# Kernel optimization log

Hardware: AMD Instinct MI355X
Metric: run time of the kernel (lower is better)

Reference implementation:

```python
import jax, jax.numpy as jnp
import numpy as np

EPS = 1e-5


def _bn(v, gamma, beta, mean, var):
    # v: [n, c, L, 1]; per-channel eval-mode batchnorm
    scale = gamma / jnp.sqrt(var + EPS)
    return v * scale[None, :, None, None] + (beta - mean * scale)[None, :, None, None]


def _conv1x1(v, w, b):
    # v: [n, c, L, 1], w: [o, c], b: [o] -> [n, o, L, 1]
    y = jnp.einsum('ncl,oc->nol', v[..., 0], w) + b[None, :, None]
    return y[..., None]


def setup_inputs() -> dict:
    key = jax.random.key(0)
    ks = jax.random.split(key, 16)
    N, C, H, W, MIP = 8, 256, 112, 112, 8
    return {
        'x': jax.random.normal(ks[0], (N, C, H, W), dtype=jnp.float32),
        'bn1_gamma': jax.random.uniform(ks[1], (C,), dtype=jnp.float32),
        'bn1_beta': jax.random.normal(ks[2], (C,), dtype=jnp.float32) * 0.1,
        'bn1_mean': jax.random.normal(ks[3], (C,), dtype=jnp.float32) * 0.1,
        'bn1_var': jax.random.uniform(ks[4], (C,), dtype=jnp.float32) + 0.5,
        'bn2_gamma': jax.random.uniform(ks[5], (C,), dtype=jnp.float32),
        'bn2_beta': jax.random.normal(ks[6], (C,), dtype=jnp.float32) * 0.1,
        'bn2_mean': jax.random.normal(ks[7], (C,), dtype=jnp.float32) * 0.1,
        'bn2_var': jax.random.uniform(ks[8], (C,), dtype=jnp.float32) + 0.5,
        'ds_w': jax.random.normal(ks[9], (MIP, C), dtype=jnp.float32) * (1.0 / np.sqrt(C)),
        'ds_b': jax.random.normal(ks[10], (MIP,), dtype=jnp.float32) * 0.01,
        'us_w': jax.random.normal(ks[11], (C, MIP), dtype=jnp.float32) * (1.0 / np.sqrt(MIP)),
        'us_b': jax.random.normal(ks[12], (C,), dtype=jnp.float32) * 0.01,
    }


def reference(x, bn1_gamma, bn1_beta, bn1_mean, bn1_var,
              bn2_gamma, bn2_beta, bn2_mean, bn2_var,
              ds_w, ds_b, us_w, us_b):
    identity = x
    # dual-axis average pooling
    x_h = jnp.mean(x, axis=3, keepdims=True)                 # [n, c, h, 1]
    x_w = jnp.mean(x, axis=2, keepdims=True).transpose(0, 1, 3, 2)  # [n, c, w, 1]
    # batchnorm (eval mode)
    x_h = _bn(x_h, bn1_gamma, bn1_beta, bn1_mean, bn1_var)
    x_w = _bn(x_w, bn2_gamma, bn2_beta, bn2_mean, bn2_var)
    # channel-reduce 1x1 conv + relu
    d_h = jax.nn.relu(_conv1x1(x_h, ds_w, ds_b))             # [n, mip, h, 1]
    d_w = jax.nn.relu(_conv1x1(x_w, ds_w, ds_b))             # [n, mip, w, 1]
    # channel-expand 1x1 conv + sigmoid
    a_h = jax.nn.sigmoid(_conv1x1(d_h, us_w, us_b))          # [n, c, h, 1]
    a_w = jax.nn.sigmoid(_conv1x1(d_w, us_w, us_b))          # [n, c, w, 1]
    a_w = a_w.transpose(0, 1, 3, 2)                          # [n, c, 1, w]
    out = identity * a_w * a_h + identity
    # h_swish: x * relu6(x + 3) / 6
    return out * jnp.clip(out + 3.0, 0.0, 6.0) * (1.0 / 6.0)
```

## Files before the change

kernel.cpp:

```cpp
#include <hip/hip_runtime.h>
#include <math.h>

#define NN 8
#define CC 256
#define HH 112
#define WW 112
#define MIP 8
#define EPS 1e-5f

__global__ __launch_bounds__(128) void pool_kernel(const float* __restrict__ x,
                                                   float* __restrict__ pool) {
    const int b = blockIdx.x;
    const int tid = threadIdx.x;
    const float* plane = x + (size_t)b * (HH * WW);

    if (tid < WW) {
        float s = 0.f;
#pragma unroll 4
        for (int h = 0; h < HH; ++h) s += plane[h * WW + tid];
        pool[(size_t)(NN * CC * HH) + (size_t)b * WW + tid] = s * (1.0f / HH);
    }
    if (tid < HH) {
        float s = 0.f;
#pragma unroll 4
        for (int w = 0; w < WW; ++w) s += plane[tid * WW + w];
        pool[(size_t)b * HH + tid] = s * (1.0f / WW);
    }
}

__global__ __launch_bounds__(256) void att_kernel(
    float* __restrict__ pool,
    const float* __restrict__ bn1_g, const float* __restrict__ bn1_b,
    const float* __restrict__ bn1_m, const float* __restrict__ bn1_v,
    const float* __restrict__ bn2_g, const float* __restrict__ bn2_b,
    const float* __restrict__ bn2_m, const float* __restrict__ bn2_v,
    const float* __restrict__ ds_w, const float* __restrict__ ds_b,
    const float* __restrict__ us_w, const float* __restrict__ us_b) {
    __shared__ float s[CC];
    __shared__ float dsh[MIP];

    const int n = blockIdx.x / HH;
    const int pos = blockIdx.x % HH;
    const int branch = blockIdx.y;
    const int c = threadIdx.x;

    const float* g  = branch ? bn2_g : bn1_g;
    const float* be = branch ? bn2_b : bn1_b;
    const float* mn = branch ? bn2_m : bn1_m;
    const float* vr = branch ? bn2_v : bn1_v;

    const size_t base = (size_t)branch * (NN * CC * HH);
    const size_t idx = base + ((size_t)(n * CC + c)) * HH + pos;

    float v = pool[idx];
    float scale = g[c] * rsqrtf(vr[c] + EPS);
    float vb = v * scale + (be[c] - mn[c] * scale);
    s[c] = vb;
    __syncthreads();

    {
        const int grp = c >> 5;
        const int l = c & 31;
        float partial = 0.f;
#pragma unroll
        for (int k = 0; k < CC / 32; ++k) {
            const int cc = l + k * 32;
            partial += ds_w[grp * CC + cc] * s[cc];
        }
#pragma unroll
        for (int off = 16; off > 0; off >>= 1)
            partial += __shfl_down(partial, off, 32);
        if (l == 0) dsh[grp] = fmaxf(partial + ds_b[grp], 0.f);
    }
    __syncthreads();

    float acc = us_b[c];
#pragma unroll
    for (int m = 0; m < MIP; ++m) acc += us_w[c * MIP + m] * dsh[m];
    float a = 1.0f / (1.0f + expf(-acc));
    pool[idx] = a;
}

__global__ __launch_bounds__(256) void apply_kernel(const float* __restrict__ x,
                                                    const float* __restrict__ att,
                                                    float* __restrict__ out) {
    const int idx = blockIdx.x * 256 + threadIdx.x;
    const int W4 = WW / 4;
    const int w4 = idx % W4;
    const int r = idx / W4;
    const int h = r % HH;
    const int nc = r / HH;

    float4 xv = ((const float4*)x)[idx];
    float ah = att[(size_t)nc * HH + h];
    float4 aw = ((const float4*)(att + (size_t)NN * CC * HH))[(size_t)nc * W4 + w4];

    float4 o;
    o.x = xv.x * (aw.x * ah) + xv.x;
    o.y = xv.y * (aw.y * ah) + xv.y;
    o.z = xv.z * (aw.z * ah) + xv.z;
    o.w = xv.w * (aw.w * ah) + xv.w;

    float4 res;
    res.x = o.x * fminf(fmaxf(o.x + 3.0f, 0.0f), 6.0f) * (1.0f / 6.0f);
    res.y = o.y * fminf(fmaxf(o.y + 3.0f, 0.0f), 6.0f) * (1.0f / 6.0f);
    res.z = o.z * fminf(fmaxf(o.z + 3.0f, 0.0f), 6.0f) * (1.0f / 6.0f);
    res.w = o.w * fminf(fmaxf(o.w + 3.0f, 0.0f), 6.0f) * (1.0f / 6.0f);

    ((float4*)out)[idx] = res;
}

extern "C" void kernel_launch(void* const* d_in, const int* in_sizes, int n_in,
                              void* d_out, int out_size, void* d_ws, size_t ws_size,
                              hipStream_t stream) {
    const float* x     = (const float*)d_in[0];
    const float* bn1_g = (const float*)d_in[1];
    const float* bn1_b = (const float*)d_in[2];
    const float* bn1_m = (const float*)d_in[3];
    const float* bn1_v = (const float*)d_in[4];
    const float* bn2_g = (const float*)d_in[5];
    const float* bn2_b = (const float*)d_in[6];
    const float* bn2_m = (const float*)d_in[7];
    const float* bn2_v = (const float*)d_in[8];
    const float* ds_w  = (const float*)d_in[9];
    const float* ds_b  = (const float*)d_in[10];
    const float* us_w  = (const float*)d_in[11];
    const float* us_b  = (const float*)d_in[12];
    float* out = (float*)d_out;
    float* pool = (float*)d_ws;

    pool_kernel<<<NN * CC, 128, 0, stream>>>(x, pool);
    att_kernel<<<dim3(NN * HH, 2), 256, 0, stream>>>(pool,
        bn1_g, bn1_b, bn1_m, bn1_v, bn2_g, bn2_b, bn2_m, bn2_v,
        ds_w, ds_b, us_w, us_b);
    const int total4 = NN * CC * HH * WW / 4;
    apply_kernel<<<total4 / 256, 256, 0, stream>>>(x, pool, out);
}
```

Before: 267.9 us.

## Stage plane tiles in LDS for pooling and transpose pooled layout to channel-last

The pool kernel now loads each (n,c) plane into shared memory with coalesced float4 loads and computes row and column means from the LDS tile. Before, it used strided global reads for the row sums. The pooled buffer layout becomes [n, pos, c], so the attention kernel reads and writes contiguously across channels. The apply kernel now runs one block per plane and caches the h and w attention vectors in shared memory. This removes the per-element gathers of attention values, at the cost of about 50KB of LDS per pool block, which limits occupancy, and strided attention reads in apply.

```diff
diff --git a/kernel.cpp b/kernel.cpp
--- a/kernel.cpp
+++ b/kernel.cpp
@@ -8,23 +8,38 @@
 #define MIP 8
 #define EPS 1e-5f
 
-__global__ __launch_bounds__(128) void pool_kernel(const float* __restrict__ x,
+
+#define TSTRIDE 113
+__global__ __launch_bounds__(256) void pool_kernel(const float* __restrict__ x,
                                                    float* __restrict__ pool) {
+    __shared__ float tile[HH * TSTRIDE];
     const int b = blockIdx.x;
+    const int n = b / CC;
+    const int c = b % CC;
     const int tid = threadIdx.x;
-    const float* plane = x + (size_t)b * (HH * WW);
 
-    if (tid < WW) {
-        float s = 0.f;
+    const float4* p4 = (const float4*)(x + (size_t)b * (HH * WW));
 #pragma unroll 4
-        for (int h = 0; h < HH; ++h) s += plane[h * WW + tid];
-        pool[(size_t)(NN * CC * HH) + (size_t)b * WW + tid] = s * (1.0f / HH);
+    for (int i = tid; i < HH * (WW / 4); i += 256) {
+        float4 v = p4[i];
+        const int h = i / (WW / 4);
+        const int w4 = i % (WW / 4);
+        float* d = &tile[h * TSTRIDE + w4 * 4];
+        d[0] = v.x; d[1] = v.y; d[2] = v.z; d[3] = v.w;
     }
+    __syncthreads();
+
     if (tid < HH) {
         float s = 0.f;
-#pragma unroll 4
-        for (int w = 0; w < WW; ++w) s += plane[tid * WW + w];
-        pool[(size_t)b * HH + tid] = s * (1.0f / WW);
+#pragma unroll 8
+        for (int w = 0; w < WW; ++w) s += tile[tid * TSTRIDE + w];
+        pool[((size_t)(n * HH + tid)) * CC + c] = s * (1.0f / WW);
+    } else if (tid >= 128 && tid < 128 + WW) {
+        const int w = tid - 128;
+        float s = 0.f;
+#pragma unroll 8
+        for (int h = 0; h < HH; ++h) s += tile[h * TSTRIDE + w];
+        pool[(size_t)(NN * HH * CC) + ((size_t)(n * WW + w)) * CC + c] = s * (1.0f / HH);
     }
 }
 
@@ -39,8 +54,6 @@
     __shared__ float s[CC];
     __shared__ float dsh[MIP];
 
-    const int n = blockIdx.x / HH;
-    const int pos = blockIdx.x % HH;
     const int branch = blockIdx.y;
     const int c = threadIdx.x;
 
@@ -49,8 +62,7 @@
     const float* mn = branch ? bn2_m : bn1_m;
     const float* vr = branch ? bn2_v : bn1_v;
 
-    const size_t base = (size_t)branch * (NN * CC * HH);
-    const size_t idx = base + ((size_t)(n * CC + c)) * HH + pos;
+    const size_t idx = (size_t)branch * (NN * HH * CC) + (size_t)blockIdx.x * CC + c;
 
     float v = pool[idx];
     float scale = g[c] * rsqrtf(vr[c] + EPS);
@@ -77,37 +89,47 @@
     float acc = us_b[c];
 #pragma unroll
     for (int m = 0; m < MIP; ++m) acc += us_w[c * MIP + m] * dsh[m];
-    float a = 1.0f / (1.0f + expf(-acc));
-    pool[idx] = a;
+    pool[idx] = 1.0f / (1.0f + expf(-acc));
 }
 
 __global__ __launch_bounds__(256) void apply_kernel(const float* __restrict__ x,
                                                     const float* __restrict__ att,
                                                     float* __restrict__ out) {
-    const int idx = blockIdx.x * 256 + threadIdx.x;
-    const int W4 = WW / 4;
-    const int w4 = idx % W4;
-    const int r = idx / W4;
-    const int h = r % HH;
-    const int nc = r / HH;
+    __shared__ float ah[HH];
+    __shared__ float aw[WW];
+    const int b = blockIdx.x;
+    const int n = b / CC;
+    const int c = b % CC;
+    const int tid = threadIdx.x;
 
-    float4 xv = ((const float4*)x)[idx];
-    float ah = att[(size_t)nc * HH + h];
-    float4 aw = ((const float4*)(att + (size_t)NN * CC * HH))[(size_t)nc * W4 + w4];
+    if (tid < HH) {
+        ah[tid] = att[((size_t)(n * HH + tid)) * CC + c];
+    } else if (tid >= 128 && tid < 128 + WW) {
+        const int w = tid - 128;
+        aw[w] = att[(size_t)(NN * HH * CC) + ((size_t)(n * WW + w)) * CC + c];
+    }
+    __syncthreads();
 
-    float4 o;
-    o.x = xv.x * (aw.x * ah) + xv.x;
-    o.y = xv.y * (aw.y * ah) + xv.y;
-    o.z = xv.z * (aw.z * ah) + xv.z;
-    o.w = xv.w * (aw.w * ah) + xv.w;
-
-    float4 res;
-    res.x = o.x * fminf(fmaxf(o.x + 3.0f, 0.0f), 6.0f) * (1.0f / 6.0f);
-    res.y = o.y * fminf(fmaxf(o.y + 3.0f, 0.0f), 6.0f) * (1.0f / 6.0f);
-    res.z = o.z * fminf(fmaxf(o.z + 3.0f, 0.0f), 6.0f) * (1.0f / 6.0f);
-    res.w = o.w * fminf(fmaxf(o.w + 3.0f, 0.0f), 6.0f) * (1.0f / 6.0f);
-
-    ((float4*)out)[idx] = res;
+    const float4* xp = (const float4*)(x + (size_t)b * (HH * WW));
+    float4* op = (float4*)(out + (size_t)b * (HH * WW));
+#pragma unroll 4
+    for (int i = tid; i < HH * (WW / 4); i += 256) {
+        const int h = i / (WW / 4);
+        const int w4 = i % (WW / 4);
+        float4 xv = xp[i];
+        const float a_h = ah[h];
+        float4 o;
+        o.x = xv.x * (aw[w4 * 4 + 0] * a_h) + xv.x;
+        o.y = xv.y * (aw[w4 * 4 + 1] * a_h) + xv.y;
+        o.z = xv.z * (aw[w4 * 4 + 2] * a_h) + xv.z;
+        o.w = xv.w * (aw[w4 * 4 + 3] * a_h) + xv.w;
+        float4 r;
+        r.x = o.x * fminf(fmaxf(o.x + 3.0f, 0.0f), 6.0f) * (1.0f / 6.0f);
+        r.y = o.y * fminf(fmaxf(o.y + 3.0f, 0.0f), 6.0f) * (1.0f / 6.0f);
+        r.z = o.z * fminf(fmaxf(o.z + 3.0f, 0.0f), 6.0f) * (1.0f / 6.0f);
+        r.w = o.w * fminf(fmaxf(o.w + 3.0f, 0.0f), 6.0f) * (1.0f / 6.0f);
+        op[i] = r;
+    }
 }
 
 extern "C" void kernel_launch(void* const* d_in, const int* in_sizes, int n_in,
@@ -129,10 +151,9 @@
     float* out = (float*)d_out;
     float* pool = (float*)d_ws;
 
-    pool_kernel<<<NN * CC, 128, 0, stream>>>(x, pool);
+    pool_kernel<<<NN * CC, 256, 0, stream>>>(x, pool);
     att_kernel<<<dim3(NN * HH, 2), 256, 0, stream>>>(pool,
         bn1_g, bn1_b, bn1_m, bn1_v, bn2_g, bn2_b, bn2_m, bn2_v,
         ds_w, ds_b, us_w, us_b);
-    const int total4 = NN * CC * HH * WW / 4;
-    apply_kernel<<<total4 / 256, 256, 0, stream>>>(x, pool, out);
+    apply_kernel<<<NN * CC, 256, 0, stream>>>(x, pool, out);
 }
```

Result: faster. 225.0 us (-16.0%).
